# Kernel optimization log

Measured on AMD Instinct MI355X. Metric: run time of the kernel, lower is better.

The kernel has to match this reference:

```python
import jax, jax.numpy as jnp
import numpy as np

DT = 0.02      # integration step (module default)
ORDER = 5      # Taylor-series order (module default)
B = 2_000_000  # batch of independent Lorenz states


def setup_inputs() -> dict:
    key = jax.random.key(0)
    x = jax.random.normal(key, (B, 3), dtype=jnp.float32)
    return {"x": x}


def _build_A(x):
    # State-dependent Lorenz Jacobian, batched: [B, 3, 3]
    x1 = x[:, 0]
    z = jnp.zeros_like(x1)
    c = lambda v: jnp.full_like(x1, v)
    row0 = jnp.stack([c(-10.0), c(10.0), z], axis=-1)
    row1 = jnp.stack([c(28.0), c(-1.0), -x1], axis=-1)
    row2 = jnp.stack([z, x1, c(-8.0 / 3.0)], axis=-1)
    return jnp.stack([row0, row1, row2], axis=1)


def reference(x):
    # F = sum_{j=0}^{ORDER} (A*dt)^j / j!   (Taylor matrix exponential), then F @ x
    A_dt = _build_A(x) * DT                                   # [B,3,3]
    I = jnp.broadcast_to(jnp.eye(3, dtype=x.dtype), A_dt.shape)
    F = I
    term = I
    for j in range(1, ORDER + 1):
        term = jnp.einsum('bij,bjk->bik', term, A_dt) / j     # term = A_dt^j / j!
        F = F + term
    return jnp.einsum('bij,bj->bi', F, x)                     # [B,3]
```

## Files before the change

kernel.cpp:

```cpp
#include <hip/hip_runtime.h>

#define LORENZ_DT 0.02f

__device__ __forceinline__ void lorenz_one(float x0, float x1, float x2,
                                           float& o0, float& o1, float& o2) {
    const float a00 = -10.0f * LORENZ_DT;
    const float a01 =  10.0f * LORENZ_DT;
    const float a10 =  28.0f * LORENZ_DT;
    const float a11 =  -1.0f * LORENZ_DT;
    const float a22 = (-8.0f / 3.0f) * LORENZ_DT;
    const float a12 = -x0 * LORENZ_DT;
    const float a21 =  x0 * LORENZ_DT;

    float t00 = 1.f, t01 = 0.f, t02 = 0.f;
    float t10 = 0.f, t11 = 1.f, t12 = 0.f;
    float t20 = 0.f, t21 = 0.f, t22 = 1.f;
    float F00 = 1.f, F01 = 0.f, F02 = 0.f;
    float F10 = 0.f, F11 = 1.f, F12 = 0.f;
    float F20 = 0.f, F21 = 0.f, F22 = 1.f;

#pragma unroll
    for (int j = 1; j <= 5; ++j) {
        const float inv = 1.0f / (float)j;
        float n00 = (t00 * a00 + t01 * a10) * inv;
        float n01 = (t00 * a01 + t01 * a11 + t02 * a21) * inv;
        float n02 = (t01 * a12 + t02 * a22) * inv;
        float n10 = (t10 * a00 + t11 * a10) * inv;
        float n11 = (t10 * a01 + t11 * a11 + t12 * a21) * inv;
        float n12 = (t11 * a12 + t12 * a22) * inv;
        float n20 = (t20 * a00 + t21 * a10) * inv;
        float n21 = (t20 * a01 + t21 * a11 + t22 * a21) * inv;
        float n22 = (t21 * a12 + t22 * a22) * inv;
        t00 = n00; t01 = n01; t02 = n02;
        t10 = n10; t11 = n11; t12 = n12;
        t20 = n20; t21 = n21; t22 = n22;
        F00 += t00; F01 += t01; F02 += t02;
        F10 += t10; F11 += t11; F12 += t12;
        F20 += t20; F21 += t21; F22 += t22;
    }

    o0 = F00 * x0 + F01 * x1 + F02 * x2;
    o1 = F10 * x0 + F11 * x1 + F12 * x2;
    o2 = F20 * x0 + F21 * x1 + F22 * x2;
}

__global__ __launch_bounds__(256) void lorenz_kernel(const float* __restrict__ x,
                                                     float* __restrict__ out, int n) {
    const int g = blockIdx.x * blockDim.x + threadIdx.x;
    const int base = g * 4;
    if (base >= n) return;

    if (base + 4 <= n) {
        const float4* xv = (const float4*)x;
        float4* ov = (float4*)out;
        float4 va = xv[g * 3 + 0];
        float4 vb = xv[g * 3 + 1];
        float4 vc = xv[g * 3 + 2];
        float xs[12] = {va.x, va.y, va.z, va.w,
                        vb.x, vb.y, vb.z, vb.w,
                        vc.x, vc.y, vc.z, vc.w};
        float os[12];
#pragma unroll
        for (int e = 0; e < 4; ++e) {
            lorenz_one(xs[e * 3 + 0], xs[e * 3 + 1], xs[e * 3 + 2],
                       os[e * 3 + 0], os[e * 3 + 1], os[e * 3 + 2]);
        }
        ov[g * 3 + 0] = make_float4(os[0], os[1], os[2], os[3]);
        ov[g * 3 + 1] = make_float4(os[4], os[5], os[6], os[7]);
        ov[g * 3 + 2] = make_float4(os[8], os[9], os[10], os[11]);
    } else {
        for (int e = base; e < n; ++e) {
            float x0 = x[e * 3 + 0], x1 = x[e * 3 + 1], x2 = x[e * 3 + 2];
            float o0, o1, o2;
            lorenz_one(x0, x1, x2, o0, o1, o2);
            out[e * 3 + 0] = o0;
            out[e * 3 + 1] = o1;
            out[e * 3 + 2] = o2;
        }
    }
}

extern "C" void kernel_launch(void* const* d_in, const int* in_sizes, int n_in,
                              void* d_out, int out_size, void* d_ws, size_t ws_size,
                              hipStream_t stream) {
    const float* x = (const float*)d_in[0];
    float* out = (float*)d_out;
    const int n = in_sizes[0] / 3;
    const int groups = (n + 3) / 4;
    const int block = 256;
    const int grid = (groups + block - 1) / block;
    lorenz_kernel<<<grid, block, 0, stream>>>(x, out, n);
}
```

Before: 76.52 us.

## Precompute Taylor polynomial coefficients at compile time and stage I/O through LDS

Since the Jacobian depends only on x0, the Taylor sum is computed symbolically at compile time as polynomials in x0. Each of the nine F entries is then evaluated with a degree-5 Horner chain instead of repeated 3x3 matrix products. Global loads and stores become fully coalesced float4 accesses staged through shared memory, with nontemporal hints. The total float count is assumed divisible by 4, which drops the scalar tail path, and the two block barriers add some synchronisation cost.

```diff
diff --git a/kernel.cpp b/kernel.cpp
--- a/kernel.cpp
+++ b/kernel.cpp
@@ -1,81 +1,110 @@
 #include <hip/hip_runtime.h>
 
-#define LORENZ_DT 0.02f
+typedef float vfloat4 __attribute__((ext_vector_type(4)));
 
-__device__ __forceinline__ void lorenz_one(float x0, float x1, float x2,
-                                           float& o0, float& o1, float& o2) {
-    const float a00 = -10.0f * LORENZ_DT;
-    const float a01 =  10.0f * LORENZ_DT;
-    const float a10 =  28.0f * LORENZ_DT;
-    const float a11 =  -1.0f * LORENZ_DT;
-    const float a22 = (-8.0f / 3.0f) * LORENZ_DT;
-    const float a12 = -x0 * LORENZ_DT;
-    const float a21 =  x0 * LORENZ_DT;
+struct PolyMat {
+    float c[3][3][6];
+};
 
-    float t00 = 1.f, t01 = 0.f, t02 = 0.f;
-    float t10 = 0.f, t11 = 1.f, t12 = 0.f;
-    float t20 = 0.f, t21 = 0.f, t22 = 1.f;
-    float F00 = 1.f, F01 = 0.f, F02 = 0.f;
-    float F10 = 0.f, F11 = 1.f, F12 = 0.f;
-    float F20 = 0.f, F21 = 0.f, F22 = 1.f;
+constexpr PolyMat compute_F() {
+    constexpr float dt = 0.02f;
+    float M[3][3][2] = {};
+    M[0][0][0] = -10.0f * dt;
+    M[0][1][0] =  10.0f * dt;
+    M[1][0][0] =  28.0f * dt;
+    M[1][1][0] =  -1.0f * dt;
+    M[1][2][1] = -dt;
+    M[2][1][1] =  dt;
+    M[2][2][0] = (-8.0f / 3.0f) * dt;
 
-#pragma unroll
+    PolyMat F = {};
+    float term[3][3][6] = {};
+    for (int i = 0; i < 3; ++i) { term[i][i][0] = 1.0f; F.c[i][i][0] = 1.0f; }
+
     for (int j = 1; j <= 5; ++j) {
-        const float inv = 1.0f / (float)j;
-        float n00 = (t00 * a00 + t01 * a10) * inv;
-        float n01 = (t00 * a01 + t01 * a11 + t02 * a21) * inv;
-        float n02 = (t01 * a12 + t02 * a22) * inv;
-        float n10 = (t10 * a00 + t11 * a10) * inv;
-        float n11 = (t10 * a01 + t11 * a11 + t12 * a21) * inv;
-        float n12 = (t11 * a12 + t12 * a22) * inv;
-        float n20 = (t20 * a00 + t21 * a10) * inv;
-        float n21 = (t20 * a01 + t21 * a11 + t22 * a21) * inv;
-        float n22 = (t21 * a12 + t22 * a22) * inv;
-        t00 = n00; t01 = n01; t02 = n02;
-        t10 = n10; t11 = n11; t12 = n12;
-        t20 = n20; t21 = n21; t22 = n22;
-        F00 += t00; F01 += t01; F02 += t02;
-        F10 += t10; F11 += t11; F12 += t12;
-        F20 += t20; F21 += t21; F22 += t22;
+        float nt[3][3][6] = {};
+        for (int i = 0; i < 3; ++i)
+            for (int k = 0; k < 3; ++k)
+                for (int m = 0; m < 3; ++m)
+                    for (int d = 0; d < 6; ++d)
+                        for (int e = 0; e < 2; ++e)
+                            if (d + e < 6)
+                                nt[i][k][d + e] += term[i][m][d] * M[m][k][e];
+        for (int i = 0; i < 3; ++i)
+            for (int k = 0; k < 3; ++k)
+                for (int d = 0; d < 6; ++d) {
+                    nt[i][k][d] /= (float)j;
+                    term[i][k][d] = nt[i][k][d];
+                    F.c[i][k][d] += nt[i][k][d];
+                }
     }
+    return F;
+}
 
-    o0 = F00 * x0 + F01 * x1 + F02 * x2;
-    o1 = F10 * x0 + F11 * x1 + F12 * x2;
-    o2 = F20 * x0 + F21 * x1 + F22 * x2;
+__device__ __forceinline__ float horner5(const float c[6], float x) {
+    float p = c[5];
+    p = fmaf(p, x, c[4]);
+    p = fmaf(p, x, c[3]);
+    p = fmaf(p, x, c[2]);
+    p = fmaf(p, x, c[1]);
+    p = fmaf(p, x, c[0]);
+    return p;
 }
 
 __global__ __launch_bounds__(256) void lorenz_kernel(const float* __restrict__ x,
-                                                     float* __restrict__ out, int n) {
-    const int g = blockIdx.x * blockDim.x + threadIdx.x;
-    const int base = g * 4;
-    if (base >= n) return;
+                                                     float* __restrict__ out, int V ) {
+    constexpr PolyMat F = compute_F();
+    __shared__ float lds[3072];
 
-    if (base + 4 <= n) {
-        const float4* xv = (const float4*)x;
-        float4* ov = (float4*)out;
-        float4 va = xv[g * 3 + 0];
-        float4 vb = xv[g * 3 + 1];
-        float4 vc = xv[g * 3 + 2];
-        float xs[12] = {va.x, va.y, va.z, va.w,
-                        vb.x, vb.y, vb.z, vb.w,
-                        vc.x, vc.y, vc.z, vc.w};
-        float os[12];
+    const int tid = threadIdx.x;
+    const int vecBase = blockIdx.x * 768;
+    const vfloat4* __restrict__ xv = (const vfloat4*)x;
+    vfloat4* __restrict__ ov = (vfloat4*)out;
+
+    vfloat4 in[3];
 #pragma unroll
-        for (int e = 0; e < 4; ++e) {
-            lorenz_one(xs[e * 3 + 0], xs[e * 3 + 1], xs[e * 3 + 2],
-                       os[e * 3 + 0], os[e * 3 + 1], os[e * 3 + 2]);
-        }
-        ov[g * 3 + 0] = make_float4(os[0], os[1], os[2], os[3]);
-        ov[g * 3 + 1] = make_float4(os[4], os[5], os[6], os[7]);
-        ov[g * 3 + 2] = make_float4(os[8], os[9], os[10], os[11]);
-    } else {
-        for (int e = base; e < n; ++e) {
-            float x0 = x[e * 3 + 0], x1 = x[e * 3 + 1], x2 = x[e * 3 + 2];
-            float o0, o1, o2;
-            lorenz_one(x0, x1, x2, o0, o1, o2);
-            out[e * 3 + 0] = o0;
-            out[e * 3 + 1] = o1;
-            out[e * 3 + 2] = o2;
+    for (int i = 0; i < 3; ++i) {
+        const int v = vecBase + i * 256 + tid;
+        in[i] = (v < V) ? __builtin_nontemporal_load(&xv[v]) : (vfloat4){0.f, 0.f, 0.f, 0.f};
+    }
+#pragma unroll
+    for (int i = 0; i < 3; ++i)
+        ((vfloat4*)lds)[i * 256 + tid] = in[i];
+    __syncthreads();
+
+    float xs[12];
+    vfloat4* myslot = (vfloat4*)(lds + tid * 12);
+#pragma unroll
+    for (int i = 0; i < 3; ++i) {
+        vfloat4 t = myslot[i];
+        xs[i * 4 + 0] = t.x; xs[i * 4 + 1] = t.y; xs[i * 4 + 2] = t.z; xs[i * 4 + 3] = t.w;
+    }
+
+    float os[12];
+#pragma unroll
+    for (int e = 0; e < 4; ++e) {
+        const float x0 = xs[e * 3 + 0];
+        const float x1 = xs[e * 3 + 1];
+        const float x2 = xs[e * 3 + 2];
+        const float f00 = horner5(F.c[0][0], x0), f01 = horner5(F.c[0][1], x0), f02 = horner5(F.c[0][2], x0);
+        const float f10 = horner5(F.c[1][0], x0), f11 = horner5(F.c[1][1], x0), f12 = horner5(F.c[1][2], x0);
+        const float f20 = horner5(F.c[2][0], x0), f21 = horner5(F.c[2][1], x0), f22 = horner5(F.c[2][2], x0);
+        os[e * 3 + 0] = fmaf(f02, x2, fmaf(f01, x1, f00 * x0));
+        os[e * 3 + 1] = fmaf(f12, x2, fmaf(f11, x1, f10 * x0));
+        os[e * 3 + 2] = fmaf(f22, x2, fmaf(f21, x1, f20 * x0));
+    }
+
+#pragma unroll
+    for (int i = 0; i < 3; ++i)
+        myslot[i] = (vfloat4){os[i * 4 + 0], os[i * 4 + 1], os[i * 4 + 2], os[i * 4 + 3]};
+    __syncthreads();
+
+#pragma unroll
+    for (int i = 0; i < 3; ++i) {
+        const int v = vecBase + i * 256 + tid;
+        if (v < V) {
+            vfloat4 t = ((vfloat4*)lds)[i * 256 + tid];
+            __builtin_nontemporal_store(t, &ov[v]);
         }
     }
 }
@@ -85,9 +114,9 @@
                               hipStream_t stream) {
     const float* x = (const float*)d_in[0];
     float* out = (float*)d_out;
-    const int n = in_sizes[0] / 3;
-    const int groups = (n + 3) / 4;
-    const int block = 256;
-    const int grid = (groups + block - 1) / block;
-    lorenz_kernel<<<grid, block, 0, stream>>>(x, out, n);
+    const int total_floats = in_sizes[0];
+    const int V = total_floats / 4;
+    const int vecs_per_block = 768;
+    const int grid = (V + vecs_per_block - 1) / vecs_per_block;
+    lorenz_kernel<<<grid, 256, 0, stream>>>(x, out, V);
 }
```

New measurement: 77.13 us. About the same (+0.8%).
